# Kernel optimization log

Measured on AMD Instinct MI355X. Metric: run time of the kernel, lower is better.

The kernel has to match this reference:

```python
import jax, jax.numpy as jnp
import numpy as np
from jax import lax

H = W = 496
K = 5            # gabor kernel size
WIN = 16         # window_size
STRIDE = 16
PATCH = 32
GAMMA = 0.5
PSI = np.pi / 2
THETAS = np.array([np.pi/8, np.pi/4, 3*np.pi/8, np.pi/2, 5*np.pi/8, 6*np.pi/8, 7*np.pi/8, np.pi], dtype=np.float32)


def setup_inputs() -> dict:
    key = jax.random.key(0)
    k1, k2, k3 = jax.random.split(key, 3)
    img = jax.random.normal(k1, (1, 1, H, W), dtype=jnp.float32)
    sigmas = jax.random.uniform(k2, (1, 3), dtype=jnp.float32) * 10.0   # nn.Parameter(rand*10)
    lambdas = jax.random.uniform(k3, (1, 3), dtype=jnp.float32) * np.pi  # nn.Parameter(rand*pi)
    return {"img": img, "sigmas": sigmas, "lambdas": lambdas}


def _gabor_bank(sigmas, lambdas):
    # axes: (sigma, lambda, theta, ky, kx)
    idx = jnp.arange(K, dtype=jnp.float32) - (K - 1) / 2.0
    sig = sigmas[0][:, None, None, None, None]          # [3,1,1,1,1]
    lam = lambdas[0][None, :, None, None, None]         # [1,3,1,1,1]
    th = jnp.asarray(THETAS)[None, None, :, None, None] # [1,1,8,1,1]
    y = idx[None, None, None, :, None]
    x = idx[None, None, None, None, :]
    sigma_x = sig
    sigma_y = sig / GAMMA
    sin_t, cos_t = jnp.sin(th), jnp.cos(th)
    y_theta = -x * sin_t + y * cos_t
    x_theta = x * cos_t + y * sin_t
    gb = jnp.exp(-0.5 * (x_theta**2 / sigma_x**2 + y_theta**2 / sigma_y**2)) \
         * jnp.cos(2.0 * np.pi * x_theta / lam + PSI)
    return gb.reshape(-1, 1, K, K)  # [72,1,5,5]


def reference(img, sigmas, lambdas):
    gb = _gabor_bank(sigmas, lambdas)
    res = lax.conv_general_dilated(
        img, gb, window_strides=(1, 1), padding=[(K // 2, K // 2)] * 2,
        dimension_numbers=("NCHW", "OIHW", "NCHW"))          # [1,72,H,W]
    res = res.reshape(1, 9, 8, H, W).max(axis=2)              # max over 8 thetas -> [1,9,H,W]
    out = res[0]                                              # [9,H,W]

    # find_maxima: per-channel threshold at 5*mean, zero below (torch.nn.Threshold)
    mean = out.mean(axis=(1, 2), keepdims=True)
    thr = jnp.where(out > mean * 5.0, out, 0.0)

    nw = H // STRIDE                                          # 31
    windows = thr.reshape(9, nw, WIN, nw, WIN).transpose(0, 1, 3, 2, 4).reshape(9, nw * nw, WIN * WIN)
    is_max = jnp.argmax(windows, axis=2) == (WIN * WIN) // 2  # [9, 961]

    w_idx = jnp.arange(nw * nw)
    rows = w_idx // nw * STRIDE + WIN // 2
    cols = w_idx % nw * STRIDE + WIN // 2

    # describe: zero-pad by 16, gather 32x32 patch at each candidate keypoint for every channel
    pad = jnp.pad(out, ((0, 0), (16, 16), (16, 16)))
    pr = rows[:, None, None] + jnp.arange(PATCH)[None, :, None]   # [961,32,1]
    pc = cols[:, None, None] + jnp.arange(PATCH)[None, None, :]   # [961,1,32]
    patches = pad[:, pr, pc]                                      # [9,961,32,32]

    # keep patches only for detected keypoints with nonzero content (original skips zero patches)
    valid_kp = jnp.any(is_max, axis=0)                            # [961]
    nonzero = jnp.any(patches != 0, axis=(2, 3))                  # [9,961]
    mask = (valid_kp[None, :] & nonzero).astype(patches.dtype)
    patches = patches * mask[:, :, None, None]
    return patches
```

## Files before the change

kernel.cpp:

```cpp
#include <hip/hip_runtime.h>
#include <math.h>

#define HH 496
#define WW 496
#define HWSZ (HH*WW)
#define NW 31
#define NWIN (NW*NW)

__constant__ float c_thetas[8] = {
    0.39269908169872414f, 0.7853981633974483f, 1.1780972450961724f,
    1.5707963267948966f,  1.9634954084936207f, 2.356194490192345f,
    2.748893571891069f,   3.141592653589793f};

__global__ void bank_kernel(const float* __restrict__ sigmas,
                            const float* __restrict__ lambdas,
                            float* __restrict__ filt,
                            float* __restrict__ meanacc) {
    int idx = threadIdx.x + blockIdx.x * blockDim.x;
    if (idx >= 1800) {
        if (idx < 1809) meanacc[(idx - 1800) * 16] = 0.0f;
        return;
    }
    int f = idx / 25, k = idx % 25;
    int dy = k / 5, dx = k % 5;
    int s = f / 24, rem = f % 24, l = rem / 8, t = rem % 8;
    float sig = sigmas[s], lam = lambdas[l], th = c_thetas[t];
    float y = (float)dy - 2.0f, x = (float)dx - 2.0f;
    float st = sinf(th), ct = cosf(th);
    float yt = -x * st + y * ct;
    float xt =  x * ct + y * st;
    float sx2 = sig * sig;
    float sy2 = 4.0f * sig * sig;
    float g = expf(-0.5f * (xt * xt / sx2 + yt * yt / sy2)) *
              cosf(6.28318530717958647692f * xt / lam + 1.5707963267948966f);
    filt[k * 72 + f] = g;
}

__global__ __launch_bounds__(256) void conv_kernel(
    const float* __restrict__ img, const float* __restrict__ filt,
    float* __restrict__ out, float* __restrict__ meanacc) {
    __shared__ float tile[20 * 20];
    __shared__ float red[4][3];
    int tid = threadIdx.x;
    int tx = tid & 15, ty = tid >> 4;
    int bx = blockIdx.x, by = blockIdx.y, cg = blockIdx.z;

    for (int i = tid; i < 400; i += 256) {
        int tY = i / 20, tX = i % 20;
        int gy = by * 16 + tY - 2, gx = bx * 16 + tX - 2;
        float v = 0.0f;
        if (gy >= 0 && gy < HH && gx >= 0 && gx < WW) v = img[gy * WW + gx];
        tile[i] = v;
    }
    __syncthreads();

    float acc[24];
#pragma unroll
    for (int f = 0; f < 24; f++) acc[f] = 0.0f;

#pragma unroll
    for (int k = 0; k < 25; k++) {
        int dy = k / 5, dx = k % 5;
        float pix = tile[(ty + dy) * 20 + (tx + dx)];
        const float* fp = filt + k * 72 + cg * 24;
#pragma unroll
        for (int f = 0; f < 24; f++) acc[f] = fmaf(pix, fp[f], acc[f]);
    }

    int y = by * 16 + ty, x = bx * 16 + tx;

    float sums[3];
#pragma unroll
    for (int cc = 0; cc < 3; cc++) {
        float maxv = acc[cc * 8];
#pragma unroll
        for (int t = 1; t < 8; t++) maxv = fmaxf(maxv, acc[cc * 8 + t]);
        out[(cg * 3 + cc) * HWSZ + y * WW + x] = maxv;
        sums[cc] = maxv;
    }

#pragma unroll
    for (int cc = 0; cc < 3; cc++) {
        float s = sums[cc];
#pragma unroll
        for (int off = 32; off > 0; off >>= 1) s += __shfl_down(s, off, 64);
        if ((tid & 63) == 0) red[tid >> 6][cc] = s;
    }
    __syncthreads();
    if (tid < 3)
        atomicAdd(&meanacc[(cg * 3 + tid) * 16],
                  red[0][tid] + red[1][tid] + red[2][tid] + red[3][tid]);
}

__global__ __launch_bounds__(256) void patch_kernel(
    const float* __restrict__ out, const float* __restrict__ meanacc,
    float* __restrict__ dst) {
    int w = blockIdx.x;
    int r = w / NW, cl = w % NW;
    int tid = threadIdx.x;
    __shared__ int lds_and[4];
    __shared__ int lds_or[4];

    int wy = tid >> 4, wx = tid & 15;
    int okmask = 0;
#pragma unroll
    for (int c = 0; c < 9; c++) {
        float m5 = meanacc[c * 16] * (5.0f / (float)HWSZ);
        float v  = out[c * HWSZ + (r * 16 + wy) * WW + (cl * 16 + wx)];
        float vc = out[c * HWSZ + (r * 16 + 8) * WW + (cl * 16 + 0)];
        float thr  = (v  > m5) ? v  : 0.0f;
        float thrc = (vc > m5) ? vc : 0.0f;
        bool ok = (tid < 128) ? (thr < thrc) : (thr <= thrc);
        okmask |= (ok ? 1 : 0) << c;
    }
#pragma unroll
    for (int off = 1; off < 64; off <<= 1) okmask &= __shfl_xor(okmask, off, 64);
    if ((tid & 63) == 0) lds_and[tid >> 6] = okmask;

    int i = tid >> 3;
    int jg = (tid & 7) << 2;
    int row = r * 16 + i - 8;
    int col = cl * 16 + jg - 8;
    bool inb = (row >= 0 && row < HH && col >= 0 && col + 3 < WW);
    float4 vals[9];
    int nzmask = 0;
#pragma unroll
    for (int c = 0; c < 9; c++) {
        float4 v = make_float4(0.f, 0.f, 0.f, 0.f);
        if (inb)
            v = *(const float4*)(out + (size_t)c * HWSZ + (size_t)row * WW + col);
        vals[c] = v;
        if (v.x != 0.f || v.y != 0.f || v.z != 0.f || v.w != 0.f) nzmask |= 1 << c;
    }
#pragma unroll
    for (int off = 1; off < 64; off <<= 1) nzmask |= __shfl_xor(nzmask, off, 64);
    if ((tid & 63) == 0) lds_or[tid >> 6] = nzmask;
    __syncthreads();

    int am = lds_and[0] & lds_and[1] & lds_and[2] & lds_and[3];
    int om = lds_or[0] | lds_or[1] | lds_or[2] | lds_or[3];
    bool valid = (am != 0);

#pragma unroll
    for (int c = 0; c < 9; c++) {
        float mk = (valid && ((om >> c) & 1)) ? 1.0f : 0.0f;
        float4 v = vals[c];
        v.x *= mk; v.y *= mk; v.z *= mk; v.w *= mk;
        *(float4*)(dst + (size_t)c * NWIN * 1024 + (size_t)w * 1024 + i * 32 + jg) = v;
    }
}

extern "C" void kernel_launch(void* const* d_in, const int* in_sizes, int n_in,
                              void* d_out, int out_size, void* d_ws, size_t ws_size,
                              hipStream_t stream) {
    const float* img     = (const float*)d_in[0];
    const float* sigmas  = (const float*)d_in[1];
    const float* lambdas = (const float*)d_in[2];
    float* ws = (float*)d_ws;
    float* filt    = ws;
    float* meanacc = ws + 2048;
    float* outb    = ws + 4096;

    bank_kernel<<<8, 256, 0, stream>>>(sigmas, lambdas, filt, meanacc);
    conv_kernel<<<dim3(NW, NW, 3), 256, 0, stream>>>(img, filt, outb, meanacc);
    patch_kernel<<<NWIN, 256, 0, stream>>>(outb, meanacc, (float*)d_out);
}
```

Measured before the change: 122.2 us.

## Fuse conv and patch kernels into one cooperative kernel with grid sync

Merges the convolution/max/mean stage and the patch extraction stage into a single cooperative launch of 961 blocks, where each block computes all 9 channels for its tile and then waits on a grid-wide barrier before thresholding and gathering patches. The center pixel values are shared through LDS instead of reloaded from global memory. This removes one kernel launch and the gap between launches, and reuses the loaded window values. In exchange each block runs three sequential conv passes, total block count drops from 2883 to 961, and a grid sync adds overhead. The cooperative launch also requires every block to be resident at once.

```diff
diff --git a/kernel.cpp b/kernel.cpp
--- a/kernel.cpp
+++ b/kernel.cpp
@@ -1,5 +1,8 @@
 #include <hip/hip_runtime.h>
+#include <hip/hip_cooperative_groups.h>
 #include <math.h>
+
+namespace cg = cooperative_groups;
 
 #define HH 496
 #define WW 496
@@ -36,14 +39,21 @@
     filt[k * 72 + f] = g;
 }
 
-__global__ __launch_bounds__(256) void conv_kernel(
+__global__ __launch_bounds__(256, 4) void fused_kernel(
     const float* __restrict__ img, const float* __restrict__ filt,
-    float* __restrict__ out, float* __restrict__ meanacc) {
+    float* __restrict__ outb, float* meanacc, float* __restrict__ dst) {
     __shared__ float tile[20 * 20];
     __shared__ float red[4][3];
+    __shared__ float centers[9];
+    __shared__ int lds_and[4];
+    __shared__ int lds_or[4];
+
+    cg::grid_group grid = cg::this_grid();
+
     int tid = threadIdx.x;
+    int w = blockIdx.x;
+    int bx = w % NW, by = w / NW;
     int tx = tid & 15, ty = tid >> 4;
-    int bx = blockIdx.x, by = blockIdx.y, cg = blockIdx.z;
 
     for (int i = tid; i < 400; i += 256) {
         int tY = i / 20, tX = i % 20;
@@ -54,62 +64,66 @@
     }
     __syncthreads();
 
-    float acc[24];
+    int y = by * 16 + ty, x = bx * 16 + tx;
+
+    for (int cg3 = 0; cg3 < 3; cg3++) {
+        float acc[24];
 #pragma unroll
-    for (int f = 0; f < 24; f++) acc[f] = 0.0f;
+        for (int f = 0; f < 24; f++) acc[f] = 0.0f;
 
 #pragma unroll
-    for (int k = 0; k < 25; k++) {
-        int dy = k / 5, dx = k % 5;
-        float pix = tile[(ty + dy) * 20 + (tx + dx)];
-        const float* fp = filt + k * 72 + cg * 24;
+        for (int k = 0; k < 25; k++) {
+            int dy = k / 5, dx = k % 5;
+            float pix = tile[(ty + dy) * 20 + (tx + dx)];
+            const float* fp = filt + k * 72 + cg3 * 24;
 #pragma unroll
-        for (int f = 0; f < 24; f++) acc[f] = fmaf(pix, fp[f], acc[f]);
+            for (int f = 0; f < 24; f++) acc[f] = fmaf(pix, fp[f], acc[f]);
+        }
+
+        float sums[3];
+#pragma unroll
+        for (int cc = 0; cc < 3; cc++) {
+            float maxv = acc[cc * 8];
+#pragma unroll
+            for (int t = 1; t < 8; t++) maxv = fmaxf(maxv, acc[cc * 8 + t]);
+            outb[(cg3 * 3 + cc) * HWSZ + y * WW + x] = maxv;
+            sums[cc] = maxv;
+        }
+
+#pragma unroll
+        for (int cc = 0; cc < 3; cc++) {
+            float s = sums[cc];
+#pragma unroll
+            for (int off = 32; off > 0; off >>= 1) s += __shfl_down(s, off, 64);
+            if ((tid & 63) == 0) red[tid >> 6][cc] = s;
+        }
+        __syncthreads();
+        if (tid < 3)
+            atomicAdd(&meanacc[(cg3 * 3 + tid) * 16],
+                      red[0][tid] + red[1][tid] + red[2][tid] + red[3][tid]);
+        __syncthreads();
     }
 
-    int y = by * 16 + ty, x = bx * 16 + tx;
+    grid.sync();
 
-    float sums[3];
+    int r = by, cl = bx;
+    int wy = tid >> 4, wx = tid & 15;
+
+    float vload[9];
 #pragma unroll
-    for (int cc = 0; cc < 3; cc++) {
-        float maxv = acc[cc * 8];
-#pragma unroll
-        for (int t = 1; t < 8; t++) maxv = fmaxf(maxv, acc[cc * 8 + t]);
-        out[(cg * 3 + cc) * HWSZ + y * WW + x] = maxv;
-        sums[cc] = maxv;
-    }
-
-#pragma unroll
-    for (int cc = 0; cc < 3; cc++) {
-        float s = sums[cc];
-#pragma unroll
-        for (int off = 32; off > 0; off >>= 1) s += __shfl_down(s, off, 64);
-        if ((tid & 63) == 0) red[tid >> 6][cc] = s;
+    for (int c = 0; c < 9; c++) {
+        vload[c] = outb[c * HWSZ + (r * 16 + wy) * WW + (cl * 16 + wx)];
+        if (tid == 128) centers[c] = vload[c];
     }
     __syncthreads();
-    if (tid < 3)
-        atomicAdd(&meanacc[(cg * 3 + tid) * 16],
-                  red[0][tid] + red[1][tid] + red[2][tid] + red[3][tid]);
-}
 
-__global__ __launch_bounds__(256) void patch_kernel(
-    const float* __restrict__ out, const float* __restrict__ meanacc,
-    float* __restrict__ dst) {
-    int w = blockIdx.x;
-    int r = w / NW, cl = w % NW;
-    int tid = threadIdx.x;
-    __shared__ int lds_and[4];
-    __shared__ int lds_or[4];
-
-    int wy = tid >> 4, wx = tid & 15;
+    volatile float* mv = meanacc;
     int okmask = 0;
 #pragma unroll
     for (int c = 0; c < 9; c++) {
-        float m5 = meanacc[c * 16] * (5.0f / (float)HWSZ);
-        float v  = out[c * HWSZ + (r * 16 + wy) * WW + (cl * 16 + wx)];
-        float vc = out[c * HWSZ + (r * 16 + 8) * WW + (cl * 16 + 0)];
-        float thr  = (v  > m5) ? v  : 0.0f;
-        float thrc = (vc > m5) ? vc : 0.0f;
+        float m5 = mv[c * 16] * (5.0f / (float)HWSZ);
+        float thr  = (vload[c]   > m5) ? vload[c]   : 0.0f;
+        float thrc = (centers[c] > m5) ? centers[c] : 0.0f;
         bool ok = (tid < 128) ? (thr < thrc) : (thr <= thrc);
         okmask |= (ok ? 1 : 0) << c;
     }
@@ -128,7 +142,7 @@
     for (int c = 0; c < 9; c++) {
         float4 v = make_float4(0.f, 0.f, 0.f, 0.f);
         if (inb)
-            v = *(const float4*)(out + (size_t)c * HWSZ + (size_t)row * WW + col);
+            v = *(const float4*)(outb + (size_t)c * HWSZ + (size_t)row * WW + col);
         vals[c] = v;
         if (v.x != 0.f || v.y != 0.f || v.z != 0.f || v.w != 0.f) nzmask |= 1 << c;
     }
@@ -160,8 +174,11 @@
     float* filt    = ws;
     float* meanacc = ws + 2048;
     float* outb    = ws + 4096;
+    float* dst     = (float*)d_out;
 
     bank_kernel<<<8, 256, 0, stream>>>(sigmas, lambdas, filt, meanacc);
-    conv_kernel<<<dim3(NW, NW, 3), 256, 0, stream>>>(img, filt, outb, meanacc);
-    patch_kernel<<<NWIN, 256, 0, stream>>>(outb, meanacc, (float*)d_out);
+
+    void* args[] = {(void*)&img, (void*)&filt, (void*)&outb, (void*)&meanacc, (void*)&dst};
+    hipLaunchCooperativeKernel((const void*)fused_kernel, dim3(NWIN), dim3(256),
+                               args, 0, stream);
 }
```

After: 234.5 us. 91.9% more time.
